# Kernel tuning notes

Hardware: AMD Instinct MI355X
Metric: run time of the kernel (lower is better)

Reference implementation:

```python
import jax, jax.numpy as jnp
import numpy as np

N_USERS = 100000
N_ITEMS = 50000
N_NODES = N_USERS + N_ITEMS
NNZ = 4000000
DIM = 64
N_LAYERS = 3
BATCH = 4096


def setup_inputs() -> dict:
    key = jax.random.key(0)
    k = jax.random.split(key, 7)
    users = jax.random.randint(k[0], (BATCH,), 0, N_USERS, dtype=jnp.int32)
    items = jax.random.randint(k[1], (BATCH,), 0, N_ITEMS, dtype=jnp.int32)
    edge_src = jax.random.randint(k[2], (NNZ,), 0, N_NODES, dtype=jnp.int32)
    edge_dst = jax.random.randint(k[3], (NNZ,), 0, N_NODES, dtype=jnp.int32)
    # normalized adjacency values (positive weights, like D^-1/2 A D^-1/2)
    edge_val = jax.random.uniform(k[4], (NNZ,), dtype=jnp.float32)
    user_emb = 0.1 * jax.random.normal(k[5], (N_USERS, DIM), dtype=jnp.float32)
    item_emb = 0.1 * jax.random.normal(k[6], (N_ITEMS, DIM), dtype=jnp.float32)
    return {"users": users, "items": items, "edge_src": edge_src,
            "edge_dst": edge_dst, "edge_val": edge_val,
            "user_emb": user_emb, "item_emb": item_emb}


def _spmm(edge_src, edge_dst, edge_val, emb):
    # y[dst] += val * emb[src]  (sparse adjacency @ dense embedding)
    vals = edge_val[:, None] * emb[edge_src]          # [nnz, d]
    return jax.ops.segment_sum(vals, edge_dst, num_segments=N_NODES)


def reference(users, items, edge_src, edge_dst, edge_val, user_emb, item_emb):
    all_emb = jnp.concatenate([user_emb, item_emb], axis=0)  # [N, d]
    acc = all_emb
    x = all_emb
    for _ in range(N_LAYERS):
        x = _spmm(edge_src, edge_dst, edge_val, x)
        acc = acc + x
    light_out = acc / jnp.asarray(N_LAYERS + 1, dtype=acc.dtype)  # layer mean
    all_users = light_out[:N_USERS]
    all_items = light_out[N_USERS:]
    u = all_users[users]                              # [B, d]
    i = all_items[items]                              # [B, d]
    scores = jnp.sum(u * i, axis=-1)                  # [B]
    return jax.nn.sigmoid(scores)
```

## Files before the change

### kernel.cpp

```cpp
#include <hip/hip_runtime.h>
#include <hip/hip_fp16.h>

#define N_USERS 100000
#define N_ITEMS 50000
#define N_NODES 150000
#define DIM 64
#define NNZ 4000000
#define BATCH 4096

#define NBUCK 586
#define CAP   7680
#define NB_C  250
#define CHUNK (NNZ / NB_C)

#define VSCALE (1.0f / 16383.0f)

typedef __half f16;

__device__ __forceinline__ float h2f(f16 h) { return __half2float(h); }

__global__ void initt_k(int* __restrict__ gticket) {
    int i = blockIdx.x * blockDim.x + threadIdx.x;
    if (i < NBUCK) gticket[i] = i * CAP;
}

__global__ __launch_bounds__(1024) void coarse_k(
        const int* __restrict__ src, const int* __restrict__ dst,
        const float* __restrict__ val, int* __restrict__ gticket,
        int2* __restrict__ ev) {
    extern __shared__ char smem[];
    int2* buf   = (int2*)smem;
    int*  hist  = (int*)(smem + (size_t)CHUNK * 8);
    int*  lbase = hist  + NBUCK;
    int*  gbase = lbase + NBUCK;
    int*  tick  = gbase + NBUCK;
    const int t  = threadIdx.x;
    const int nt = blockDim.x;
    const int lo = blockIdx.x * CHUNK;
    const int hi = lo + CHUNK;

    for (int i = t; i < NBUCK; i += nt) { hist[i] = 0; tick[i] = 0; }
    __syncthreads();
    for (int e = lo + 4 * t; e < hi; e += 4 * nt) {
        int4 d4 = *reinterpret_cast<const int4*>(&dst[e]);
        atomicAdd(&hist[d4.x >> 8], 1);
        atomicAdd(&hist[d4.y >> 8], 1);
        atomicAdd(&hist[d4.z >> 8], 1);
        atomicAdd(&hist[d4.w >> 8], 1);
    }
    __syncthreads();
    if (t < 64) {
        int lane = t;
        int carry = 0;
        for (int c = 0; c < (NBUCK + 63) / 64; ++c) {
            int idx = c * 64 + lane;
            int v = (idx < NBUCK) ? hist[idx] : 0;
            int s = v;
            #pragma unroll
            for (int off = 1; off < 64; off <<= 1) {
                int u = __shfl_up(s, off, 64);
                if (lane >= off) s += u;
            }
            if (idx < NBUCK) lbase[idx] = carry + s - v;
            carry += __shfl(s, 63, 64);
        }
    }
    for (int i = t; i < NBUCK; i += nt)
        gbase[i] = atomicAdd(&gticket[i], hist[i]);
    __syncthreads();
    for (int e = lo + 4 * t; e < hi; e += 4 * nt) {
        int4   d4 = *reinterpret_cast<const int4*>(&dst[e]);
        int4   s4 = *reinterpret_cast<const int4*>(&src[e]);
        float4 v4 = *reinterpret_cast<const float4*>(&val[e]);
        int bk, p;
        bk = d4.x >> 8; p = lbase[bk] + atomicAdd(&tick[bk], 1);
        buf[p] = make_int2(s4.x | ((d4.x & 255) << 18), __float_as_int(v4.x));
        bk = d4.y >> 8; p = lbase[bk] + atomicAdd(&tick[bk], 1);
        buf[p] = make_int2(s4.y | ((d4.y & 255) << 18), __float_as_int(v4.y));
        bk = d4.z >> 8; p = lbase[bk] + atomicAdd(&tick[bk], 1);
        buf[p] = make_int2(s4.z | ((d4.z & 255) << 18), __float_as_int(v4.z));
        bk = d4.w >> 8; p = lbase[bk] + atomicAdd(&tick[bk], 1);
        buf[p] = make_int2(s4.w | ((d4.w & 255) << 18), __float_as_int(v4.w));
    }
    __syncthreads();
    int wid = t >> 6, lane = t & 63, nw = nt >> 6;
    for (int bk = wid; bk < NBUCK; bk += nw) {
        int cnt = hist[bk], lb = lbase[bk], gb = gbase[bk];
        for (int i = lane; i < cnt; i += 64)
            ev[gb + i] = buf[lb + i];
    }
}

__global__ void scanC_k(const int* __restrict__ gticket, int* __restrict__ bktbase) {
    __shared__ int sh[1024];
    int tid = threadIdx.x;
    int v = (tid < NBUCK) ? (gticket[tid] - tid * CAP) : 0;
    sh[tid] = v;
    __syncthreads();
    for (int off = 1; off < 1024; off <<= 1) {
        int t = (tid >= off) ? sh[tid - off] : 0;
        __syncthreads();
        sh[tid] += t;
        __syncthreads();
    }
    if (tid < NBUCK) bktbase[tid] = sh[tid] - v;
}

__global__ void fine_k(const int* __restrict__ gticket, const int* __restrict__ bktbase,
                       const int2* __restrict__ ev,
                       uint* __restrict__ sorted, int* __restrict__ row) {
    __shared__ int hist[256];
    __shared__ int sh[256];
    int k = blockIdx.x, t = threadIdx.x;
    hist[t] = 0;
    __syncthreads();
    int cnt = gticket[k] - k * CAP;
    int s0  = k * CAP;
    for (int i = t; i < cnt; i += 256)
        atomicAdd(&hist[(ev[s0 + i].x >> 18) & 255], 1);
    __syncthreads();
    int v = hist[t];
    sh[t] = v;
    __syncthreads();
    for (int off = 1; off < 256; off <<= 1) {
        int tmp = (t >= off) ? sh[t - off] : 0;
        __syncthreads();
        sh[t] += tmp;
        __syncthreads();
    }
    int excl    = sh[t] - v;
    int rowbase = bktbase[k];
    int node    = (k << 8) + t;
    if (node < N_NODES) row[node] = rowbase + excl;
    if (k == 0 && t == 0) row[N_NODES] = NNZ;
    hist[t] = excl;
    __syncthreads();
    for (int i = t; i < cnt; i += 256) {
        int2 r = ev[s0 + i];
        int p  = atomicAdd(&hist[(r.x >> 18) & 255], 1);
        float vf = __int_as_float(r.y);
        int q = (int)(vf * 16383.0f + 0.5f);
        q = q < 0 ? 0 : (q > 16383 ? 16383 : q);
        sorted[rowbase + p] = (uint)(r.x & 0x3FFFF) | ((uint)q << 18);
    }
}

__global__ void conv_k(const float4* __restrict__ ue, const float4* __restrict__ ie,
                       ushort4* __restrict__ X0) {
    int i = blockIdx.x * blockDim.x + threadIdx.x;
    const int total  = N_NODES * DIM / 4;
    const int ubound = N_USERS * DIM / 4;
    if (i >= total) return;
    float4 v = (i < ubound) ? ue[i] : ie[i - ubound];
    f16 a = __float2half(v.x), b = __float2half(v.y);
    f16 c = __float2half(v.z), d = __float2half(v.w);
    ushort4 o;
    o.x = *reinterpret_cast<ushort*>(&a);
    o.y = *reinterpret_cast<ushort*>(&b);
    o.z = *reinterpret_cast<ushort*>(&c);
    o.w = *reinterpret_cast<ushort*>(&d);
    X0[i] = o;
}

__global__ void gather16_k(const int* __restrict__ row, const uint* __restrict__ se,
                           const uint2* __restrict__ X4, uint2* __restrict__ Y4) {
    int wid  = (blockIdx.x * blockDim.x + threadIdx.x) >> 6;
    int lane = threadIdx.x & 63;
    if (wid >= N_NODES) return;
    int sub  = lane >> 4;
    int quad = lane & 15;
    int beg = row[wid], end = row[wid + 1];
    half2 acc0 = __floats2half2_rn(0.f, 0.f);
    half2 acc1 = acc0;
    for (int base = beg; base < end; base += 64) {
        int rem = end - base;
        int n = rem < 64 ? rem : 64;
        uint evu = 0u;
        if (lane < n) evu = se[base + lane];
        int ng = (n + 3) >> 2;
        for (int g0 = 0; g0 < ng; g0 += 4) {
            uint2 xr[4]; float vs[4];
            #pragma unroll
            for (int k = 0; k < 4; ++k) {
                int ei = ((g0 + k) << 2) + sub;
                uint r = (uint)__shfl((int)evu, ei, 64);
                vs[k]  = (float)(r >> 18) * VSCALE;
                xr[k]  = X4[((size_t)(r & 0x3FFFFu) << 4) + quad];
            }
            #pragma unroll
            for (int k = 0; k < 4; ++k) {
                half2 vh = __float2half2_rn(vs[k]);
                acc0 = __hfma2(*reinterpret_cast<half2*>(&xr[k].x), vh, acc0);
                acc1 = __hfma2(*reinterpret_cast<half2*>(&xr[k].y), vh, acc1);
            }
        }
    }
    float2 f0 = __half22float2(acc0);
    float2 f1 = __half22float2(acc1);
    float a0 = f0.x, a1 = f0.y, a2 = f1.x, a3 = f1.y;
    a0 += __shfl_xor(a0, 16, 64);  a1 += __shfl_xor(a1, 16, 64);
    a2 += __shfl_xor(a2, 16, 64);  a3 += __shfl_xor(a3, 16, 64);
    a0 += __shfl_xor(a0, 32, 64);  a1 += __shfl_xor(a1, 32, 64);
    a2 += __shfl_xor(a2, 32, 64);  a3 += __shfl_xor(a3, 32, 64);
    if (sub == 0) {
        half2 h0 = __floats2half2_rn(a0, a1);
        half2 h1 = __floats2half2_rn(a2, a3);
        uint2 o;
        o.x = *reinterpret_cast<uint*>(&h0);
        o.y = *reinterpret_cast<uint*>(&h1);
        Y4[((size_t)wid << 4) + quad] = o;
    }
}

__global__ void gather3_k(const int* __restrict__ users, const int* __restrict__ items,
                          const int* __restrict__ row, const uint* __restrict__ se,
                          const f16* __restrict__ X, f16* __restrict__ X3p) {
    int s    = (blockIdx.x * blockDim.x + threadIdx.x) >> 6;
    int lane = threadIdx.x & 63;
    if (s >= 2 * BATCH) return;
    int wid = (s < BATCH) ? users[s] : (N_USERS + items[s - BATCH]);
    int beg = row[wid], end = row[wid + 1];
    float acc = 0.f;
    for (int base = beg; base < end; base += 64) {
        int rem = end - base;
        int n = rem < 64 ? rem : 64;
        uint evu = 0u;
        if (lane < n) evu = se[base + lane];
        int n8 = (n + 7) & ~7;
        for (int j = 0; j < n8; j += 8) {
            float xv[8], vv[8];
            #pragma unroll
            for (int k = 0; k < 8; ++k) {
                uint r = (uint)__shfl((int)evu, j + k, 64);
                vv[k] = (float)(r >> 18) * VSCALE;
                xv[k] = h2f(X[((r & 0x3FFFFu) << 6) + lane]);
            }
            #pragma unroll
            for (int k = 0; k < 8; ++k) acc += vv[k] * xv[k];
        }
    }
    X3p[(s << 6) + lane] = __float2half(acc);
}

__global__ void final_k(const int* __restrict__ users, const int* __restrict__ items,
                        const float* __restrict__ ue, const float* __restrict__ ie,
                        const f16* __restrict__ X1, const f16* __restrict__ X2,
                        const f16* __restrict__ X3p, float* __restrict__ out) {
    int b    = blockIdx.x * (blockDim.x / 64) + (threadIdx.x / 64);
    int lane = threadIdx.x & 63;
    if (b >= BATCH) return;
    int u  = users[b];
    int it = items[b];
    int uo = (u << 6) + lane;
    int io = ((N_USERS + it) << 6) + lane;
    float au = ue[uo]               + h2f(X1[uo]) + h2f(X2[uo]) + h2f(X3p[(b << 6) + lane]);
    float ai = ie[(it << 6) + lane] + h2f(X1[io]) + h2f(X2[io]) + h2f(X3p[((b + BATCH) << 6) + lane]);
    float p = au * ai * (1.0f / 16.0f);
    #pragma unroll
    for (int off = 32; off; off >>= 1) p += __shfl_down(p, off, 64);
    if (lane == 0) out[b] = 1.0f / (1.0f + __expf(-p));
}

extern "C" void kernel_launch(void* const* d_in, const int* in_sizes, int n_in,
                              void* d_out, int out_size, void* d_ws, size_t ws_size,
                              hipStream_t stream) {
    const int*   users = (const int*)  d_in[0];
    const int*   items = (const int*)  d_in[1];
    const int*   esrc  = (const int*)  d_in[2];
    const int*   edst  = (const int*)  d_in[3];
    const float* eval  = (const float*)d_in[4];
    const float* uemb  = (const float*)d_in[5];
    const float* iemb  = (const float*)d_in[6];
    float*       out   = (float*)      d_out;

    const size_t XB = (size_t)N_NODES * DIM * sizeof(f16);
    char* ws = (char*)d_ws;
    f16*  X0     = (f16*) (ws);
    f16*  X1     = (f16*) (ws + XB);
    f16*  X2     = (f16*) (ws + 2 * XB);
    f16*  X3p    = (f16*) (ws + 3 * XB);
    uint* sorted = (uint*)(ws + 3 * XB + ((size_t)2 * BATCH * DIM * 2 + 255 & ~255UL));
    char* p      = (char*)sorted + (size_t)NNZ * sizeof(uint);
    int*  row     = (int*)(p);                 p += ((size_t)(N_NODES + 1) * 4 + 255) & ~255UL;
    int*  gticket = (int*)(p);                 p += (NBUCK * 4 + 255) & ~255UL;
    int*  bktbase = (int*)(p);                 p += (NBUCK * 4 + 255) & ~255UL;
    int2* cev = (int2*)(ws);

    const size_t CLDS = (size_t)CHUNK * 8 + (size_t)4 * NBUCK * 4;
    hipFuncSetAttribute((const void*)coarse_k,
                        hipFuncAttributeMaxDynamicSharedMemorySize, (int)CLDS);

    initt_k<<<(NBUCK + 255) / 256, 256, 0, stream>>>(gticket);
    coarse_k<<<NB_C, 1024, CLDS, stream>>>(esrc, edst, eval, gticket, cev);
    scanC_k<<<1, 1024, 0, stream>>>(gticket, bktbase);
    fine_k<<<NBUCK, 256, 0, stream>>>(gticket, bktbase, cev, sorted, row);

    conv_k<<<(N_NODES * DIM / 4 + 255) / 256, 256, 0, stream>>>(
        (const float4*)uemb, (const float4*)iemb, (ushort4*)X0);

    const int gthreads = N_NODES * 64;
    gather16_k<<<(gthreads + 255) / 256, 256, 0, stream>>>(row, sorted,
                                                           (const uint2*)X0, (uint2*)X1);
    gather16_k<<<(gthreads + 255) / 256, 256, 0, stream>>>(row, sorted,
                                                           (const uint2*)X1, (uint2*)X2);
    gather3_k<<<(2 * BATCH * 64 + 255) / 256, 256, 0, stream>>>(users, items, row,
                                                                sorted, X2, X3p);

    final_k<<<(BATCH * 64 + 255) / 256, 256, 0, stream>>>(users, items, uemb, iemb,
                                                          X1, X2, X3p, out);
}
```

Before: 219.0 us.

## Compute second propagation layer only for nodes needed by the batch

Adds a marking kernel that flags the batch user/item nodes and every source neighbour of their rows. The second full-graph gather then skips unflagged rows, since only those rows of X2 feed the final batch-only third layer. The third-layer gather is also fused into the final scoring kernel, which removes the X3p buffer and one launch. With random edges and an average in-degree near 27, most nodes still get flagged, so the skip may be modest. The added memset and marking kernel cost time of their own.

Result: no change. 216.0 us (-1.4%).

```diff
diff --git a/kernel.cpp b/kernel.cpp
--- a/kernel.cpp
+++ b/kernel.cpp
@@ -160,6 +160,19 @@
     o.z = *reinterpret_cast<ushort*>(&c);
     o.w = *reinterpret_cast<ushort*>(&d);
     X0[i] = o;
+}
+
+__global__ void mark2_k(const int* __restrict__ users, const int* __restrict__ items,
+                        const int* __restrict__ row, const uint* __restrict__ se,
+                        unsigned char* __restrict__ need2) {
+    int s    = (blockIdx.x * blockDim.x + threadIdx.x) >> 6;
+    int lane = threadIdx.x & 63;
+    if (s >= 2 * BATCH) return;
+    int wid = (s < BATCH) ? users[s] : (N_USERS + items[s - BATCH]);
+    if (lane == 0) need2[wid] = 1;
+    int beg = row[wid], end = row[wid + 1];
+    for (int i = beg + lane; i < end; i += 64)
+        need2[se[i] & 0x3FFFFu] = 1;
 }
 
 __global__ void gather16_k(const int* __restrict__ row, const uint* __restrict__ se,
@@ -212,13 +225,61 @@
     }
 }
 
-__global__ void gather3_k(const int* __restrict__ users, const int* __restrict__ items,
-                          const int* __restrict__ row, const uint* __restrict__ se,
-                          const f16* __restrict__ X, f16* __restrict__ X3p) {
-    int s    = (blockIdx.x * blockDim.x + threadIdx.x) >> 6;
+__global__ void gather16m_k(const int* __restrict__ row, const uint* __restrict__ se,
+                            const uint2* __restrict__ X4, uint2* __restrict__ Y4,
+                            const unsigned char* __restrict__ need2) {
+    int wid  = (blockIdx.x * blockDim.x + threadIdx.x) >> 6;
     int lane = threadIdx.x & 63;
-    if (s >= 2 * BATCH) return;
-    int wid = (s < BATCH) ? users[s] : (N_USERS + items[s - BATCH]);
+    if (wid >= N_NODES) return;
+    if (!need2[wid]) return;
+    int sub  = lane >> 4;
+    int quad = lane & 15;
+    int beg = row[wid], end = row[wid + 1];
+    half2 acc0 = __floats2half2_rn(0.f, 0.f);
+    half2 acc1 = acc0;
+    for (int base = beg; base < end; base += 64) {
+        int rem = end - base;
+        int n = rem < 64 ? rem : 64;
+        uint evu = 0u;
+        if (lane < n) evu = se[base + lane];
+        int ng = (n + 3) >> 2;
+        for (int g0 = 0; g0 < ng; g0 += 4) {
+            uint2 xr[4]; float vs[4];
+            #pragma unroll
+            for (int k = 0; k < 4; ++k) {
+                int ei = ((g0 + k) << 2) + sub;
+                uint r = (uint)__shfl((int)evu, ei, 64);
+                vs[k]  = (float)(r >> 18) * VSCALE;
+                xr[k]  = X4[((size_t)(r & 0x3FFFFu) << 4) + quad];
+            }
+            #pragma unroll
+            for (int k = 0; k < 4; ++k) {
+                half2 vh = __float2half2_rn(vs[k]);
+                acc0 = __hfma2(*reinterpret_cast<half2*>(&xr[k].x), vh, acc0);
+                acc1 = __hfma2(*reinterpret_cast<half2*>(&xr[k].y), vh, acc1);
+            }
+        }
+    }
+    float2 f0 = __half22float2(acc0);
+    float2 f1 = __half22float2(acc1);
+    float a0 = f0.x, a1 = f0.y, a2 = f1.x, a3 = f1.y;
+    a0 += __shfl_xor(a0, 16, 64);  a1 += __shfl_xor(a1, 16, 64);
+    a2 += __shfl_xor(a2, 16, 64);  a3 += __shfl_xor(a3, 16, 64);
+    a0 += __shfl_xor(a0, 32, 64);  a1 += __shfl_xor(a1, 32, 64);
+    a2 += __shfl_xor(a2, 32, 64);  a3 += __shfl_xor(a3, 32, 64);
+    if (sub == 0) {
+        half2 h0 = __floats2half2_rn(a0, a1);
+        half2 h1 = __floats2half2_rn(a2, a3);
+        uint2 o;
+        o.x = *reinterpret_cast<uint*>(&h0);
+        o.y = *reinterpret_cast<uint*>(&h1);
+        Y4[((size_t)wid << 4) + quad] = o;
+    }
+}
+
+__device__ __forceinline__ float row_gather_acc(int wid, const int* __restrict__ row,
+                                                const uint* __restrict__ se,
+                                                const f16* __restrict__ X, int lane) {
     int beg = row[wid], end = row[wid + 1];
     float acc = 0.f;
     for (int base = beg; base < end; base += 64) {
@@ -239,22 +300,27 @@
             for (int k = 0; k < 8; ++k) acc += vv[k] * xv[k];
         }
     }
-    X3p[(s << 6) + lane] = __float2half(acc);
-}
-
-__global__ void final_k(const int* __restrict__ users, const int* __restrict__ items,
-                        const float* __restrict__ ue, const float* __restrict__ ie,
-                        const f16* __restrict__ X1, const f16* __restrict__ X2,
-                        const f16* __restrict__ X3p, float* __restrict__ out) {
+    return acc;
+}
+
+__global__ void final2_k(const int* __restrict__ users, const int* __restrict__ items,
+                         const float* __restrict__ ue, const float* __restrict__ ie,
+                         const int* __restrict__ row, const uint* __restrict__ se,
+                         const f16* __restrict__ X1, const f16* __restrict__ X2,
+                         float* __restrict__ out) {
     int b    = blockIdx.x * (blockDim.x / 64) + (threadIdx.x / 64);
     int lane = threadIdx.x & 63;
     if (b >= BATCH) return;
     int u  = users[b];
     int it = items[b];
-    int uo = (u << 6) + lane;
-    int io = ((N_USERS + it) << 6) + lane;
-    float au = ue[uo]               + h2f(X1[uo]) + h2f(X2[uo]) + h2f(X3p[(b << 6) + lane]);
-    float ai = ie[(it << 6) + lane] + h2f(X1[io]) + h2f(X2[io]) + h2f(X3p[((b + BATCH) << 6) + lane]);
+    int un = u;
+    int in = N_USERS + it;
+    int uo = (un << 6) + lane;
+    int io = (in << 6) + lane;
+    float x3u = row_gather_acc(un, row, se, X2, lane);
+    float x3i = row_gather_acc(in, row, se, X2, lane);
+    float au = ue[uo]               + h2f(X1[uo]) + h2f(X2[uo]) + x3u;
+    float ai = ie[(it << 6) + lane] + h2f(X1[io]) + h2f(X2[io]) + x3i;
     float p = au * ai * (1.0f / 16.0f);
     #pragma unroll
     for (int off = 32; off; off >>= 1) p += __shfl_down(p, off, 64);
@@ -278,12 +344,12 @@
     f16*  X0     = (f16*) (ws);
     f16*  X1     = (f16*) (ws + XB);
     f16*  X2     = (f16*) (ws + 2 * XB);
-    f16*  X3p    = (f16*) (ws + 3 * XB);
-    uint* sorted = (uint*)(ws + 3 * XB + ((size_t)2 * BATCH * DIM * 2 + 255 & ~255UL));
+    uint* sorted = (uint*)(ws + 3 * XB);
     char* p      = (char*)sorted + (size_t)NNZ * sizeof(uint);
     int*  row     = (int*)(p);                 p += ((size_t)(N_NODES + 1) * 4 + 255) & ~255UL;
     int*  gticket = (int*)(p);                 p += (NBUCK * 4 + 255) & ~255UL;
     int*  bktbase = (int*)(p);                 p += (NBUCK * 4 + 255) & ~255UL;
+    unsigned char* need2 = (unsigned char*)(p);
     int2* cev = (int2*)(ws);
 
     const size_t CLDS = (size_t)CHUNK * 8 + (size_t)4 * NBUCK * 4;
@@ -298,14 +364,16 @@
     conv_k<<<(N_NODES * DIM / 4 + 255) / 256, 256, 0, stream>>>(
         (const float4*)uemb, (const float4*)iemb, (ushort4*)X0);
 
+    hipMemsetAsync(need2, 0, N_NODES, stream);
+    mark2_k<<<(2 * BATCH * 64 + 255) / 256, 256, 0, stream>>>(users, items, row,
+                                                              sorted, need2);
+
     const int gthreads = N_NODES * 64;
     gather16_k<<<(gthreads + 255) / 256, 256, 0, stream>>>(row, sorted,
                                                            (const uint2*)X0, (uint2*)X1);
-    gather16_k<<<(gthreads + 255) / 256, 256, 0, stream>>>(row, sorted,
-                                                           (const uint2*)X1, (uint2*)X2);
-    gather3_k<<<(2 * BATCH * 64 + 255) / 256, 256, 0, stream>>>(users, items, row,
-                                                                sorted, X2, X3p);
-
-    final_k<<<(BATCH * 64 + 255) / 256, 256, 0, stream>>>(users, items, uemb, iemb,
-                                                          X1, X2, X3p, out);
-}
+    gather16m_k<<<(gthreads + 255) / 256, 256, 0, stream>>>(row, sorted,
+                                                            (const uint2*)X1, (uint2*)X2,
+                                                            need2);
+    final2_k<<<(BATCH * 64 + 255) / 256, 256, 0, stream>>>(users, items, uemb, iemb,
+                                                           row, sorted, X1, X2, out);
+}
```

## Skip layer-2 rows not needed by batch, fuse layer-3 gather into final

Applied to the files above, without the earlier changes.

A new marking kernel flags the batch user and item nodes and all their in-neighbors. The second propagation layer then computes only the flagged rows, since only those feed the final scores. The third-layer row gathers are folded into the scoring kernel, which removes the X3p buffer and one launch. The gather inner loop is also unrolled from 4 to 8 edge groups to keep more loads in flight. The trade-offs are an added memset and marking pass, and higher register use from the wider unroll.

Result: faster. 214.7 us (-2.0%).

```diff
diff --git a/kernel.cpp b/kernel.cpp
--- a/kernel.cpp
+++ b/kernel.cpp
@@ -162,11 +162,27 @@
     X0[i] = o;
 }
 
+__global__ void mark2_k(const int* __restrict__ users, const int* __restrict__ items,
+                        const int* __restrict__ row, const uint* __restrict__ se,
+                        unsigned char* __restrict__ need2) {
+    int s    = (blockIdx.x * blockDim.x + threadIdx.x) >> 6;
+    int lane = threadIdx.x & 63;
+    if (s >= 2 * BATCH) return;
+    int wid = (s < BATCH) ? users[s] : (N_USERS + items[s - BATCH]);
+    if (lane == 0) need2[wid] = 1;
+    int beg = row[wid], end = row[wid + 1];
+    for (int i = beg + lane; i < end; i += 64)
+        need2[se[i] & 0x3FFFFu] = 1;
+}
+
+template <bool MASKED>
 __global__ void gather16_k(const int* __restrict__ row, const uint* __restrict__ se,
-                           const uint2* __restrict__ X4, uint2* __restrict__ Y4) {
+                           const uint2* __restrict__ X4, uint2* __restrict__ Y4,
+                           const unsigned char* __restrict__ need2) {
     int wid  = (blockIdx.x * blockDim.x + threadIdx.x) >> 6;
     int lane = threadIdx.x & 63;
     if (wid >= N_NODES) return;
+    if (MASKED && !need2[wid]) return;
     int sub  = lane >> 4;
     int quad = lane & 15;
     int beg = row[wid], end = row[wid + 1];
@@ -178,17 +194,17 @@
         uint evu = 0u;
         if (lane < n) evu = se[base + lane];
         int ng = (n + 3) >> 2;
-        for (int g0 = 0; g0 < ng; g0 += 4) {
-            uint2 xr[4]; float vs[4];
-            #pragma unroll
-            for (int k = 0; k < 4; ++k) {
+        for (int g0 = 0; g0 < ng; g0 += 8) {
+            uint2 xr[8]; float vs[8];
+            #pragma unroll
+            for (int k = 0; k < 8; ++k) {
                 int ei = ((g0 + k) << 2) + sub;
                 uint r = (uint)__shfl((int)evu, ei, 64);
                 vs[k]  = (float)(r >> 18) * VSCALE;
                 xr[k]  = X4[((size_t)(r & 0x3FFFFu) << 4) + quad];
             }
             #pragma unroll
-            for (int k = 0; k < 4; ++k) {
+            for (int k = 0; k < 8; ++k) {
                 half2 vh = __float2half2_rn(vs[k]);
                 acc0 = __hfma2(*reinterpret_cast<half2*>(&xr[k].x), vh, acc0);
                 acc1 = __hfma2(*reinterpret_cast<half2*>(&xr[k].y), vh, acc1);
@@ -212,13 +228,9 @@
     }
 }
 
-__global__ void gather3_k(const int* __restrict__ users, const int* __restrict__ items,
-                          const int* __restrict__ row, const uint* __restrict__ se,
-                          const f16* __restrict__ X, f16* __restrict__ X3p) {
-    int s    = (blockIdx.x * blockDim.x + threadIdx.x) >> 6;
-    int lane = threadIdx.x & 63;
-    if (s >= 2 * BATCH) return;
-    int wid = (s < BATCH) ? users[s] : (N_USERS + items[s - BATCH]);
+__device__ __forceinline__ float row_gather_acc(int wid, const int* __restrict__ row,
+                                                const uint* __restrict__ se,
+                                                const f16* __restrict__ X, int lane) {
     int beg = row[wid], end = row[wid + 1];
     float acc = 0.f;
     for (int base = beg; base < end; base += 64) {
@@ -239,22 +251,27 @@
             for (int k = 0; k < 8; ++k) acc += vv[k] * xv[k];
         }
     }
-    X3p[(s << 6) + lane] = __float2half(acc);
-}
-
-__global__ void final_k(const int* __restrict__ users, const int* __restrict__ items,
-                        const float* __restrict__ ue, const float* __restrict__ ie,
-                        const f16* __restrict__ X1, const f16* __restrict__ X2,
-                        const f16* __restrict__ X3p, float* __restrict__ out) {
+    return acc;
+}
+
+__global__ void final2_k(const int* __restrict__ users, const int* __restrict__ items,
+                         const float* __restrict__ ue, const float* __restrict__ ie,
+                         const int* __restrict__ row, const uint* __restrict__ se,
+                         const f16* __restrict__ X1, const f16* __restrict__ X2,
+                         float* __restrict__ out) {
     int b    = blockIdx.x * (blockDim.x / 64) + (threadIdx.x / 64);
     int lane = threadIdx.x & 63;
     if (b >= BATCH) return;
     int u  = users[b];
     int it = items[b];
-    int uo = (u << 6) + lane;
-    int io = ((N_USERS + it) << 6) + lane;
-    float au = ue[uo]               + h2f(X1[uo]) + h2f(X2[uo]) + h2f(X3p[(b << 6) + lane]);
-    float ai = ie[(it << 6) + lane] + h2f(X1[io]) + h2f(X2[io]) + h2f(X3p[((b + BATCH) << 6) + lane]);
+    int un = u;
+    int in = N_USERS + it;
+    int uo = (un << 6) + lane;
+    int io = (in << 6) + lane;
+    float x3u = row_gather_acc(un, row, se, X2, lane);
+    float x3i = row_gather_acc(in, row, se, X2, lane);
+    float au = ue[uo]               + h2f(X1[uo]) + h2f(X2[uo]) + x3u;
+    float ai = ie[(it << 6) + lane] + h2f(X1[io]) + h2f(X2[io]) + x3i;
     float p = au * ai * (1.0f / 16.0f);
     #pragma unroll
     for (int off = 32; off; off >>= 1) p += __shfl_down(p, off, 64);
@@ -278,12 +295,12 @@
     f16*  X0     = (f16*) (ws);
     f16*  X1     = (f16*) (ws + XB);
     f16*  X2     = (f16*) (ws + 2 * XB);
-    f16*  X3p    = (f16*) (ws + 3 * XB);
-    uint* sorted = (uint*)(ws + 3 * XB + ((size_t)2 * BATCH * DIM * 2 + 255 & ~255UL));
+    uint* sorted = (uint*)(ws + 3 * XB);
     char* p      = (char*)sorted + (size_t)NNZ * sizeof(uint);
     int*  row     = (int*)(p);                 p += ((size_t)(N_NODES + 1) * 4 + 255) & ~255UL;
     int*  gticket = (int*)(p);                 p += (NBUCK * 4 + 255) & ~255UL;
     int*  bktbase = (int*)(p);                 p += (NBUCK * 4 + 255) & ~255UL;
+    unsigned char* need2 = (unsigned char*)(p);
     int2* cev = (int2*)(ws);
 
     const size_t CLDS = (size_t)CHUNK * 8 + (size_t)4 * NBUCK * 4;
@@ -298,14 +315,15 @@
     conv_k<<<(N_NODES * DIM / 4 + 255) / 256, 256, 0, stream>>>(
         (const float4*)uemb, (const float4*)iemb, (ushort4*)X0);
 
+    hipMemsetAsync(need2, 0, N_NODES, stream);
+    mark2_k<<<(2 * BATCH * 64 + 255) / 256, 256, 0, stream>>>(users, items, row,
+                                                              sorted, need2);
+
     const int gthreads = N_NODES * 64;
-    gather16_k<<<(gthreads + 255) / 256, 256, 0, stream>>>(row, sorted,
-                                                           (const uint2*)X0, (uint2*)X1);
-    gather16_k<<<(gthreads + 255) / 256, 256, 0, stream>>>(row, sorted,
-                                                           (const uint2*)X1, (uint2*)X2);
-    gather3_k<<<(2 * BATCH * 64 + 255) / 256, 256, 0, stream>>>(users, items, row,
-                                                                sorted, X2, X3p);
-
-    final_k<<<(BATCH * 64 + 255) / 256, 256, 0, stream>>>(users, items, uemb, iemb,
-                                                          X1, X2, X3p, out);
-}
+    gather16_k<false><<<(gthreads + 255) / 256, 256, 0, stream>>>(
+        row, sorted, (const uint2*)X0, (uint2*)X1, need2);
+    gather16_k<true><<<(gthreads + 255) / 256, 256, 0, stream>>>(
+        row, sorted, (const uint2*)X1, (uint2*)X2, need2);
+    final2_k<<<(BATCH * 64 + 255) / 256, 256, 0, stream>>>(users, items, uemb, iemb,
+                                                           row, sorted, X1, X2, out);
+}
```
